# Performance work log

Hardware: AMD Instinct MI355X
Metric: run time of the kernel (lower is better)

## Reference

```python
import jax, jax.numpy as jnp
import numpy as np

B, L, D_FEAT = 16, 2048, 512
H, D_HID, UNITS = 8, 512, 512


def setup_inputs() -> dict:
    key = jax.random.key(0)
    ks = jax.random.split(key, 8)
    s_feat = 1.0 / np.sqrt(D_FEAT)
    s_hid = 1.0 / np.sqrt(D_HID)
    s_u = 1.0 / np.sqrt(UNITS)
    return {
        "features": jax.random.normal(ks[0], (B, L, D_FEAT), jnp.float32),
        "hidden": jax.random.normal(ks[1], (B, H, D_HID), jnp.float32),
        # Per-head Dense params stacked along a leading head axis.
        "W1": jax.random.normal(ks[2], (H, D_FEAT, UNITS), jnp.float32) * s_feat,
        "b1": jnp.zeros((H, UNITS), jnp.float32),
        "W2": jax.random.normal(ks[3], (H, D_HID, UNITS), jnp.float32) * s_hid,
        "b2": jnp.zeros((H, UNITS), jnp.float32),
        "V": jax.random.normal(ks[4], (H, UNITS), jnp.float32) * s_u,
        "bV": jnp.zeros((H,), jnp.float32),
    }


def reference(features, hidden, W1, b1, W2, b2, V, bV):
    # features: [B, L, Df]; hidden: [B, H, Dh]
    # Per-head: tanh(W1(features) + W2(hidden_h)) -> V -> softmax over L -> weighted sum.
    f_proj = jnp.einsum("bld,hdu->bhlu", features, W1) + b1[None, :, None, :]   # [B,H,L,U]
    h_proj = jnp.einsum("bhd,hdu->bhu", hidden, W2) + b2[None, :, :]            # [B,H,U]
    act = jnp.tanh(f_proj + h_proj[:, :, None, :])                               # [B,H,L,U]
    score = jnp.einsum("bhlu,hu->bhl", act, V) + bV[None, :, None]               # [B,H,L]
    attn = jax.nn.softmax(score, axis=-1)                                        # softmax over L
    context = jnp.einsum("bhl,bld->bhd", attn, features)                         # [B,H,Df]
    # Original stacks weights (each [B,L,1]) along axis=2 -> [B,L,H,1]
    attention_weights = jnp.transpose(attn, (0, 2, 1))[..., None]                # [B,L,H,1]
    return context, attention_weights
```

## Files before the change

### kernel.cpp

```cpp
#include <hip/hip_runtime.h>
#include <hip/hip_bf16.h>

#define B_ 16
#define L_ 2048
#define DF 512
#define H_ 8
#define DH 512
#define U_ 512

typedef unsigned short u16;
typedef __attribute__((ext_vector_type(8))) short bf16x8;
typedef __attribute__((ext_vector_type(4))) float f32x4;

__device__ __forceinline__ u16 f2bf(float x) {
  __hip_bfloat16 h = __float2bfloat16(x);
  u16 u;
  __builtin_memcpy(&u, &h, 2);
  return u;
}

__device__ __forceinline__ void load_lds16(const void* g, void* l) {
  __builtin_amdgcn_global_load_lds(
      (const __attribute__((address_space(1))) void*)g,
      (__attribute__((address_space(3))) void*)l, 16, 0, 0);
}

__device__ __forceinline__ float fast_tanh2(float x) {
  float e = __expf(2.f * x);
  return 1.f - __fdividef(2.f, e + 1.f);
}

__global__ __launch_bounds__(256) void convert_kernel(
    const float* __restrict__ F, u16* __restrict__ Abf,
    const float* __restrict__ W1, u16* __restrict__ W1T) {
  __shared__ float t[32][33];
  if (blockIdx.x < 16384) {
    size_t i = ((size_t)blockIdx.x * 256 + threadIdx.x) * 4;
    float4 v = *(const float4*)(F + i);
    ushort4 o;
    o.x = f2bf(v.x); o.y = f2bf(v.y); o.z = f2bf(v.z); o.w = f2bf(v.w);
    *(ushort4*)(Abf + i) = o;
  } else {
    int bid = blockIdx.x - 16384;
    int d0 = (bid & 15) * 32, u0 = ((bid >> 4) & 15) * 32, h = bid >> 8;
    const float* src = W1 + (size_t)h * DF * U_;
    u16* dst = W1T + (size_t)h * U_ * DF;
#pragma unroll
    for (int i = 0; i < 4; ++i) {
      int idx = threadIdx.x + i * 256;
      int r = idx >> 5, c = idx & 31;
      t[r][c] = src[(size_t)(d0 + r) * U_ + u0 + c];
    }
    __syncthreads();
#pragma unroll
    for (int i = 0; i < 4; ++i) {
      int idx = threadIdx.x + i * 256;
      int r = idx >> 5, c = idx & 31;
      dst[(size_t)(u0 + r) * DF + d0 + c] = f2bf(t[c][r]);
    }
  }
}

__global__ __launch_bounds__(128) void hproj_part_kernel(
    const float* __restrict__ hidden, const float* __restrict__ W2,
    float* __restrict__ partial) {
  int h = blockIdx.x;
  int u = blockIdx.y * 128 + threadIdx.x;
  int d0 = blockIdx.z * 64;
  __shared__ float hs[B_][64];
  for (int idx = threadIdx.x; idx < B_ * 64; idx += 128) {
    int b = idx >> 6, d = idx & 63;
    hs[b][d] = hidden[(size_t)(b * H_ + h) * DH + d0 + d];
  }
  __syncthreads();
  float acc[B_];
#pragma unroll
  for (int b = 0; b < B_; b++) acc[b] = 0.f;
  const float* w2p = W2 + ((size_t)h * DH + d0) * U_ + u;
  for (int d = 0; d < 64; d++) {
    float w = w2p[(size_t)d * U_];
#pragma unroll
    for (int b = 0; b < B_; b++) acc[b] += hs[b][d] * w;
  }
#pragma unroll
  for (int b = 0; b < B_; b++)
    partial[(((size_t)blockIdx.z * B_ + b) * H_ + h) * U_ + u] = acc[b];
}

__global__ __launch_bounds__(256) void hproj_combine_kernel(
    const float* __restrict__ partial, const float* __restrict__ b1,
    const float* __restrict__ b2, float* __restrict__ c) {
  int i = blockIdx.x * 256 + threadIdx.x;
  int hu = i & (H_ * U_ - 1);
  float s = b1[hu] + b2[hu];
#pragma unroll
  for (int z = 0; z < 8; z++) s += partial[(size_t)z * B_ * H_ * U_ + i];
  c[i] = s;
}

#define BKQ 32

__global__ __launch_bounds__(512, 2) void score_kernel(
    const u16* __restrict__ Abf, const u16* __restrict__ W1T,
    const float* __restrict__ C, const float* __restrict__ V,
    float* __restrict__ pscore) {
  int bid = blockIdx.x;
  int logical = (bid & 7) * 256 + (bid >> 3);
  int mt = logical >> 4;
  int hu = logical & 15;
  int h = hu & 7, ut = hu >> 3;
  int b = mt >> 3;
  int l0 = (mt & 7) * 256;
  int u0 = ut * 256;

  int tid = threadIdx.x;
  int lane = tid & 63, wid = tid >> 6;
  int wr = wid >> 2, wc = wid & 3;
  int rl = lane & 15, q = lane >> 4;

  __shared__ u16 As[4][256 * BKQ];
  __shared__ u16 Bs[4][256 * BKQ];
  __shared__ float redsm[4][256];

  const u16* Fb = Abf + ((size_t)b * L_ + l0) * DF;
  const u16* Wh = W1T + ((size_t)h * U_ + u0) * DF;

  float cu[4], vv[4];
#pragma unroll
  for (int n = 0; n < 4; ++n) {
    int col = u0 + wc * 64 + n * 16 + rl;
    cu[n] = C[(size_t)(b * H_ + h) * U_ + col];
    vv[n] = V[h * U_ + col];
  }
  f32x4 acc[8][4];
#pragma unroll
  for (int m = 0; m < 8; ++m)
#pragma unroll
    for (int n = 0; n < 4; ++n)
#pragma unroll
      for (int j = 0; j < 4; ++j) acc[m][n][j] = cu[n];

#define STAGE(bufi, kb)                                                    \
  {                                                                        \
    _Pragma("unroll") for (int i_ = 0; i_ < 2; ++i_) {                     \
      int idx_ = i_ * 512 + tid;                                           \
      int row_ = idx_ >> 2;                                                \
      int ke_ = ((idx_ & 3) ^ ((row_ >> 1) & 3)) << 3;                     \
      load_lds16(Fb + ((size_t)row_ << 9) + (kb) + ke_,                    \
                 &As[bufi][idx_ * 8]);                                     \
    }                                                                      \
    _Pragma("unroll") for (int i_ = 0; i_ < 2; ++i_) {                     \
      int idx_ = i_ * 512 + tid;                                           \
      int row_ = idx_ >> 2;                                                \
      int ke_ = ((idx_ & 3) ^ ((row_ >> 1) & 3)) << 3;                     \
      load_lds16(Wh + ((size_t)row_ << 9) + (kb) + ke_,                    \
                 &Bs[bufi][idx_ * 8]);                                     \
    }                                                                      \
  }

#define COMPUTE(bufi)                                                      \
  {                                                                        \
    bf16x8 bF[4];                                                          \
    _Pragma("unroll") for (int n = 0; n < 4; ++n) {                        \
      int rB = wc * 64 + n * 16 + rl;                                      \
      bF[n] = *(const bf16x8*)&Bs[bufi][(rB << 5) +                        \
                                        ((q ^ ((rB >> 1) & 3)) << 3)];     \
    }                                                                      \
    _Pragma("unroll") for (int m = 0; m < 8; ++m) {                        \
      int rA = wr * 128 + m * 16 + rl;                                     \
      bf16x8 aF = *(const bf16x8*)&As[bufi][(rA << 5) +                    \
                                           ((q ^ ((rA >> 1) & 3)) << 3)];  \
      _Pragma("unroll") for (int n = 0; n < 4; ++n)                        \
        acc[m][n] = __builtin_amdgcn_mfma_f32_16x16x32_bf16(               \
            aF, bF[n], acc[m][n], 0, 0, 0);                                \
    }                                                                      \
  }

  STAGE(0, 0);
  STAGE(1, BKQ);
  STAGE(2, 2 * BKQ);

#pragma unroll 1
  for (int t = 0; t < 13; ++t) {
    STAGE((t + 3) & 3, (t + 3) * BKQ);
    asm volatile("s_waitcnt vmcnt(12)" ::: "memory");
    __builtin_amdgcn_s_barrier();
    COMPUTE(t & 3);
    asm volatile("s_waitcnt lgkmcnt(0)" ::: "memory");
    __builtin_amdgcn_s_barrier();
  }
  asm volatile("s_waitcnt vmcnt(8)" ::: "memory");
  __builtin_amdgcn_s_barrier();
  COMPUTE(1);
  asm volatile("s_waitcnt lgkmcnt(0)" ::: "memory");
  __builtin_amdgcn_s_barrier();
  asm volatile("s_waitcnt vmcnt(4)" ::: "memory");
  __builtin_amdgcn_s_barrier();
  COMPUTE(2);
  asm volatile("s_waitcnt lgkmcnt(0)" ::: "memory");
  __builtin_amdgcn_s_barrier();
  asm volatile("s_waitcnt vmcnt(0)" ::: "memory");
  __builtin_amdgcn_s_barrier();
  COMPUTE(3);
#undef STAGE
#undef COMPUTE

  float part[32];
#pragma unroll
  for (int m = 0; m < 8; ++m)
#pragma unroll
    for (int j = 0; j < 4; ++j) {
      float s = 0.f;
#pragma unroll
      for (int n = 0; n < 4; ++n) s += fast_tanh2(acc[m][n][j]) * vv[n];
      part[m * 4 + j] = s;
    }
#pragma unroll
  for (int p = 0; p < 32; ++p) {
    float v = part[p];
    v += __shfl_xor(v, 1, 64);
    v += __shfl_xor(v, 2, 64);
    v += __shfl_xor(v, 4, 64);
    v += __shfl_xor(v, 8, 64);
    part[p] = v;
  }
  __syncthreads();
  if (rl == 0) {
#pragma unroll
    for (int m = 0; m < 8; ++m)
#pragma unroll
      for (int j = 0; j < 4; ++j)
        redsm[wc][wr * 128 + m * 16 + q * 4 + j] = part[m * 4 + j];
  }
  __syncthreads();
  if (tid < 256) {
    float s = redsm[0][tid] + redsm[1][tid] + redsm[2][tid] + redsm[3][tid];
    pscore[((size_t)ut * B_ * H_ + b * H_ + h) * L_ + l0 + tid] = s;
  }
}

__global__ __launch_bounds__(256) void softmax_kernel(
    const float* __restrict__ pscore, float* __restrict__ attn,
    float* __restrict__ aw_out) {
  int bh = blockIdx.x;
  int b = bh / H_, h = bh % H_;
  const float* p0 = pscore + (size_t)bh * L_;
  const float* p1 = pscore + ((size_t)B_ * H_ + bh) * L_;
  __shared__ float sv[L_];
  __shared__ float red[256];

  for (int i = threadIdx.x; i < L_ / 4; i += 256) {
    float4 a = ((const float4*)p0)[i];
    float4 c = ((const float4*)p1)[i];
    a.x += c.x; a.y += c.y; a.z += c.z; a.w += c.w;
    ((float4*)sv)[i] = a;
  }
  __syncthreads();

  float m = -1e30f;
  for (int l = threadIdx.x; l < L_; l += 256) m = fmaxf(m, sv[l]);
  red[threadIdx.x] = m;
  __syncthreads();
  for (int st = 128; st > 0; st >>= 1) {
    if (threadIdx.x < st)
      red[threadIdx.x] = fmaxf(red[threadIdx.x], red[threadIdx.x + st]);
    __syncthreads();
  }
  m = red[0];
  __syncthreads();

  float sum = 0.f;
  for (int l = threadIdx.x; l < L_; l += 256) sum += __expf(sv[l] - m);
  red[threadIdx.x] = sum;
  __syncthreads();
  for (int st = 128; st > 0; st >>= 1) {
    if (threadIdx.x < st) red[threadIdx.x] += red[threadIdx.x + st];
    __syncthreads();
  }
  float inv = 1.f / red[0];

  for (int l = threadIdx.x; l < L_; l += 256) {
    float a = __expf(sv[l] - m) * inv;
    attn[(size_t)bh * L_ + l] = a;
    aw_out[((size_t)b * L_ + l) * H_ + h] = a;
  }
}

__global__ __launch_bounds__(256) void context_part_kernel(
    const float* __restrict__ F, const float* __restrict__ attn,
    float* __restrict__ partial) {
  int b = blockIdx.x;
  int d0 = blockIdx.y * 64;
  int lz = blockIdx.z;
  int td = threadIdx.x & 63;
  int tl = threadIdx.x >> 6;

  __shared__ float as[H_][256];
  for (int idx = threadIdx.x; idx < H_ * 256; idx += 256)
    as[idx >> 8][idx & 255] =
        attn[((size_t)b * H_ + (idx >> 8)) * L_ + lz * 256 + (idx & 255)];
  __syncthreads();

  float acc[H_] = {};
  for (int l = tl; l < 256; l += 4) {
    float f = F[((size_t)b * L_ + lz * 256 + l) * DF + d0 + td];
#pragma unroll
    for (int h = 0; h < H_; h++) acc[h] += as[h][l] * f;
  }

  __shared__ float red[4][H_][64];
#pragma unroll
  for (int h = 0; h < H_; h++) red[tl][h][td] = acc[h];
  __syncthreads();
  if (tl == 0) {
#pragma unroll
    for (int h = 0; h < H_; h++) {
      float v = red[0][h][td] + red[1][h][td] + red[2][h][td] + red[3][h][td];
      partial[(size_t)lz * B_ * H_ * DF + ((size_t)b * H_ + h) * DF + d0 + td] =
          v;
    }
  }
}

__global__ __launch_bounds__(256) void context_combine_kernel(
    const float* __restrict__ partial, float* __restrict__ ctx_out) {
  int i = blockIdx.x * 256 + threadIdx.x;
  float s = 0.f;
#pragma unroll
  for (int z = 0; z < 8; z++) s += partial[(size_t)z * B_ * H_ * DF + i];
  ctx_out[i] = s;
}

extern "C" void kernel_launch(void* const* d_in, const int* in_sizes, int n_in,
                              void* d_out, int out_size, void* d_ws,
                              size_t ws_size, hipStream_t stream) {
  const float* features = (const float*)d_in[0];
  const float* hidden   = (const float*)d_in[1];
  const float* W1       = (const float*)d_in[2];
  const float* b1       = (const float*)d_in[3];
  const float* W2       = (const float*)d_in[4];
  const float* b2       = (const float*)d_in[5];
  const float* V        = (const float*)d_in[6];

  float* out = (float*)d_out;
  float* ctx_out = out;
  float* aw_out  = out + B_ * H_ * DF;

  float* c_buf  = (float*)d_ws;
  float* pscore = c_buf + (size_t)B_ * H_ * U_;
  float* attn   = pscore;
  float* hpart  = pscore;
  float* cpart  = pscore + (size_t)2 * B_ * H_ * L_;
  u16* Abf = (u16*)(cpart + (size_t)8 * B_ * H_ * DF);
  u16* W1T = Abf + (size_t)B_ * L_ * DF;

  convert_kernel<<<16384 + 2048, 256, 0, stream>>>(features, Abf, W1, W1T);
  hproj_part_kernel<<<dim3(H_, U_ / 128, 8), 128, 0, stream>>>(hidden, W2,
                                                               hpart);
  hproj_combine_kernel<<<(B_ * H_ * U_) / 256, 256, 0, stream>>>(hpart, b1, b2,
                                                                 c_buf);
  score_kernel<<<2048, 512, 0, stream>>>(Abf, W1T, c_buf, V, pscore);
  softmax_kernel<<<B_ * H_, 256, 0, stream>>>(pscore, attn, aw_out);
  context_part_kernel<<<dim3(B_, DF / 64, 8), 256, 0, stream>>>(features, attn,
                                                                cpart);
  context_combine_kernel<<<(B_ * H_ * DF) / 256, 256, 0, stream>>>(cpart,
                                                                   ctx_out);
}
```

Measured before the change: 268.7 us.

## Make score GEMM persistent with BK=64 double-buffered pipeline, fuse hproj into prep

The score kernel becomes persistent: 256 blocks each walk all eight L-tiles of one batch, head and U-half, using a BK=64 double-buffered LDS pipeline. Global-to-LDS loads are interleaved with MFMA quarter-steps, and the tanh/V reduction runs at each tile boundary. The hidden projection is merged into the conversion kernel to save a launch, and the context kernel reads the bf16 features instead of fp32 to halve its traffic. Risks: only 256 blocks, about one per CU, which may cut latency hiding; the context sum loses precision from the bf16 inputs.

```diff
diff --git a/kernel.cpp b/kernel.cpp
--- a/kernel.cpp
+++ b/kernel.cpp
@@ -19,6 +19,13 @@
   return u;
 }
 
+__device__ __forceinline__ float bf2f(u16 u) {
+  unsigned x = ((unsigned)u) << 16;
+  float f;
+  __builtin_memcpy(&f, &x, 4);
+  return f;
+}
+
 __device__ __forceinline__ void load_lds16(const void* g, void* l) {
   __builtin_amdgcn_global_load_lds(
       (const __attribute__((address_space(1))) void*)g,
@@ -30,17 +37,20 @@
   return 1.f - __fdividef(2.f, e + 1.f);
 }
 
-__global__ __launch_bounds__(256) void convert_kernel(
+__global__ __launch_bounds__(256) void prep_kernel(
     const float* __restrict__ F, u16* __restrict__ Abf,
-    const float* __restrict__ W1, u16* __restrict__ W1T) {
+    const float* __restrict__ W1, u16* __restrict__ W1T,
+    const float* __restrict__ hidden, const float* __restrict__ W2,
+    float* __restrict__ hpart) {
   __shared__ float t[32][33];
+  __shared__ float hs[B_][64];
   if (blockIdx.x < 16384) {
     size_t i = ((size_t)blockIdx.x * 256 + threadIdx.x) * 4;
     float4 v = *(const float4*)(F + i);
     ushort4 o;
     o.x = f2bf(v.x); o.y = f2bf(v.y); o.z = f2bf(v.z); o.w = f2bf(v.w);
     *(ushort4*)(Abf + i) = o;
-  } else {
+  } else if (blockIdx.x < 18432) {
     int bid = blockIdx.x - 16384;
     int d0 = (bid & 15) * 32, u0 = ((bid >> 4) & 15) * 32, h = bid >> 8;
     const float* src = W1 + (size_t)h * DF * U_;
@@ -58,33 +68,29 @@
       int r = idx >> 5, c = idx & 31;
       dst[(size_t)(u0 + r) * DF + d0 + c] = f2bf(t[c][r]);
     }
-  }
-}
-
-__global__ __launch_bounds__(128) void hproj_part_kernel(
-    const float* __restrict__ hidden, const float* __restrict__ W2,
-    float* __restrict__ partial) {
-  int h = blockIdx.x;
-  int u = blockIdx.y * 128 + threadIdx.x;
-  int d0 = blockIdx.z * 64;
-  __shared__ float hs[B_][64];
-  for (int idx = threadIdx.x; idx < B_ * 64; idx += 128) {
-    int b = idx >> 6, d = idx & 63;
-    hs[b][d] = hidden[(size_t)(b * H_ + h) * DH + d0 + d];
-  }
-  __syncthreads();
-  float acc[B_];
-#pragma unroll
-  for (int b = 0; b < B_; b++) acc[b] = 0.f;
-  const float* w2p = W2 + ((size_t)h * DH + d0) * U_ + u;
-  for (int d = 0; d < 64; d++) {
-    float w = w2p[(size_t)d * U_];
-#pragma unroll
-    for (int b = 0; b < B_; b++) acc[b] += hs[b][d] * w;
-  }
-#pragma unroll
-  for (int b = 0; b < B_; b++)
-    partial[(((size_t)blockIdx.z * B_ + b) * H_ + h) * U_ + u] = acc[b];
+  } else {
+    int bid = blockIdx.x - 18432;
+    int h = bid & 7, uy = (bid >> 3) & 1, dz = bid >> 4;
+    int u = uy * 256 + threadIdx.x;
+    int d0 = dz * 64;
+    for (int idx = threadIdx.x; idx < B_ * 64; idx += 256) {
+      int b = idx >> 6, d = idx & 63;
+      hs[b][d] = hidden[(size_t)(b * H_ + h) * DH + d0 + d];
+    }
+    __syncthreads();
+    float acc[B_];
+#pragma unroll
+    for (int b = 0; b < B_; b++) acc[b] = 0.f;
+    const float* w2p = W2 + ((size_t)h * DH + d0) * U_ + u;
+    for (int d = 0; d < 64; d++) {
+      float w = w2p[(size_t)d * U_];
+#pragma unroll
+      for (int b = 0; b < B_; b++) acc[b] += hs[b][d] * w;
+    }
+#pragma unroll
+    for (int b = 0; b < B_; b++)
+      hpart[(((size_t)dz * B_ + b) * H_ + h) * U_ + u] = acc[b];
+  }
 }
 
 __global__ __launch_bounds__(256) void hproj_combine_kernel(
@@ -98,19 +104,14 @@
   c[i] = s;
 }
 
-#define BKQ 32
-
 __global__ __launch_bounds__(512, 2) void score_kernel(
     const u16* __restrict__ Abf, const u16* __restrict__ W1T,
     const float* __restrict__ C, const float* __restrict__ V,
     float* __restrict__ pscore) {
   int bid = blockIdx.x;
-  int logical = (bid & 7) * 256 + (bid >> 3);
-  int mt = logical >> 4;
-  int hu = logical & 15;
-  int h = hu & 7, ut = hu >> 3;
-  int b = mt >> 3;
-  int l0 = (mt & 7) * 256;
+  int xcd = bid & 7, slot = bid >> 3;
+  int h = slot & 7, ut = (slot >> 3) & 1, mg = slot >> 4;
+  int b = xcd * 2 + mg;
   int u0 = ut * 256;
 
   int tid = threadIdx.x;
@@ -118,11 +119,11 @@
   int wr = wid >> 2, wc = wid & 3;
   int rl = lane & 15, q = lane >> 4;
 
-  __shared__ u16 As[4][256 * BKQ];
-  __shared__ u16 Bs[4][256 * BKQ];
+  __shared__ u16 As[2][256 * 64];
+  __shared__ u16 Bs[2][256 * 64];
   __shared__ float redsm[4][256];
 
-  const u16* Fb = Abf + ((size_t)b * L_ + l0) * DF;
+  const u16* FbB = Abf + (size_t)b * L_ * DF;
   const u16* Wh = W1T + ((size_t)h * U_ + u0) * DF;
 
   float cu[4], vv[4];
@@ -140,103 +141,136 @@
 #pragma unroll
       for (int j = 0; j < 4; ++j) acc[m][n][j] = cu[n];
 
-#define STAGE(bufi, kb)                                                    \
+#define SA_(bi, hf, l0v, kb)                                               \
   {                                                                        \
     _Pragma("unroll") for (int i_ = 0; i_ < 2; ++i_) {                     \
-      int idx_ = i_ * 512 + tid;                                           \
-      int row_ = idx_ >> 2;                                                \
-      int ke_ = ((idx_ & 3) ^ ((row_ >> 1) & 3)) << 3;                     \
-      load_lds16(Fb + ((size_t)row_ << 9) + (kb) + ke_,                    \
-                 &As[bufi][idx_ * 8]);                                     \
+      int idx_ = (hf)*1024 + i_ * 512 + tid;                               \
+      int row_ = idx_ >> 3;                                                \
+      int ke_ = ((idx_ & 7) ^ (row_ & 7)) << 3;                            \
+      load_lds16(FbB + (((size_t)((l0v) + row_)) << 9) + (kb) + ke_,       \
+                 &As[bi][idx_ * 8]);                                       \
     }                                                                      \
+  }
+#define SB_(bi, hf, kb)                                                    \
+  {                                                                        \
     _Pragma("unroll") for (int i_ = 0; i_ < 2; ++i_) {                     \
-      int idx_ = i_ * 512 + tid;                                           \
-      int row_ = idx_ >> 2;                                                \
-      int ke_ = ((idx_ & 3) ^ ((row_ >> 1) & 3)) << 3;                     \
-      load_lds16(Wh + ((size_t)row_ << 9) + (kb) + ke_,                    \
-                 &Bs[bufi][idx_ * 8]);                                     \
+      int idx_ = (hf)*1024 + i_ * 512 + tid;                               \
+      int row_ = idx_ >> 3;                                                \
+      int ke_ = ((idx_ & 7) ^ (row_ & 7)) << 3;                            \
+      load_lds16(Wh + (((size_t)row_) << 9) + (kb) + ke_,                  \
+                 &Bs[bi][idx_ * 8]);                                       \
     }                                                                      \
   }
-
-#define COMPUTE(bufi)                                                      \
+#define RD_A(mh, ks, bi)                                                   \
   {                                                                        \
-    bf16x8 bF[4];                                                          \
-    _Pragma("unroll") for (int n = 0; n < 4; ++n) {                        \
-      int rB = wc * 64 + n * 16 + rl;                                      \
-      bF[n] = *(const bf16x8*)&Bs[bufi][(rB << 5) +                        \
-                                        ((q ^ ((rB >> 1) & 3)) << 3)];     \
+    _Pragma("unroll") for (int mm = 0; mm < 4; ++mm) {                     \
+      int rA = wr * 128 + ((mh)*4 + mm) * 16 + rl;                         \
+      aF[mm] = *(const bf16x8*)&As[bi][(rA << 6) +                         \
+                                       ((((ks)*4 + q) ^ (rA & 7)) << 3)];  \
     }                                                                      \
-    _Pragma("unroll") for (int m = 0; m < 8; ++m) {                        \
-      int rA = wr * 128 + m * 16 + rl;                                     \
-      bf16x8 aF = *(const bf16x8*)&As[bufi][(rA << 5) +                    \
-                                           ((q ^ ((rA >> 1) & 3)) << 3)];  \
-      _Pragma("unroll") for (int n = 0; n < 4; ++n)                        \
-        acc[m][n] = __builtin_amdgcn_mfma_f32_16x16x32_bf16(               \
-            aF, bF[n], acc[m][n], 0, 0, 0);                                \
+  }
+#define RD_B(ks, bi)                                                       \
+  {                                                                        \
+    _Pragma("unroll") for (int nn = 0; nn < 4; ++nn) {                     \
+      int rB = wc * 64 + nn * 16 + rl;                                     \
+      bF[nn] = *(const bf16x8*)&Bs[bi][(rB << 6) +                         \
+                                       ((((ks)*4 + q) ^ (rB & 7)) << 3)];  \
     }                                                                      \
   }
-
-  STAGE(0, 0);
-  STAGE(1, BKQ);
-  STAGE(2, 2 * BKQ);
+#define MMQ(mh)                                                            \
+  {                                                                        \
+    _Pragma("unroll") for (int mm = 0; mm < 4; ++mm)                       \
+    _Pragma("unroll") for (int nn = 0; nn < 4; ++nn)                       \
+      acc[(mh)*4 + mm][nn] = __builtin_amdgcn_mfma_f32_16x16x32_bf16(      \
+          aF[mm], bF[nn], acc[(mh)*4 + mm][nn], 0, 0, 0);                  \
+  }
+
+  SA_(0, 0, 0, 0);
+  SB_(0, 0, 0);
+  SB_(0, 1, 0);
+  SA_(0, 1, 0, 0);
+  asm volatile("s_waitcnt vmcnt(2)" ::: "memory");
+  __builtin_amdgcn_s_barrier();
+  __builtin_amdgcn_sched_barrier(0);
 
 #pragma unroll 1
-  for (int t = 0; t < 13; ++t) {
-    STAGE((t + 3) & 3, (t + 3) * BKQ);
-    asm volatile("s_waitcnt vmcnt(12)" ::: "memory");
+  for (int g = 0; g < 64; ++g) {
+    int cc = g & 1, nb = cc ^ 1;
+    int l0 = (g >> 3) * 256;
+    int l0n = ((g + 1) >> 3) * 256;
+    int kbn = ((g + 1) & 7) * 64;
+    bf16x8 aF[4], bF[4];
+    RD_A(0, 0, cc);
+    RD_B(0, cc);
+    if (g < 63) SA_(nb, 0, l0n, kbn);
+    MMQ(0);
+    if (g < 63)
+      asm volatile("s_waitcnt vmcnt(2)" ::: "memory");
+    else
+      asm volatile("s_waitcnt vmcnt(0)" ::: "memory");
     __builtin_amdgcn_s_barrier();
-    COMPUTE(t & 3);
+    __builtin_amdgcn_sched_barrier(0);
+    RD_A(1, 0, cc);
+    if (g < 63) SB_(nb, 0, kbn);
+    MMQ(1);
+    RD_A(0, 1, cc);
+    RD_B(1, cc);
+    if (g < 63) SB_(nb, 1, kbn);
+    MMQ(0);
+    RD_A(1, 1, cc);
+    if (g < 63) SA_(nb, 1, l0n, kbn);
+    MMQ(1);
     asm volatile("s_waitcnt lgkmcnt(0)" ::: "memory");
+    asm volatile("s_waitcnt vmcnt(2)" ::: "memory");
     __builtin_amdgcn_s_barrier();
-  }
-  asm volatile("s_waitcnt vmcnt(8)" ::: "memory");
-  __builtin_amdgcn_s_barrier();
-  COMPUTE(1);
-  asm volatile("s_waitcnt lgkmcnt(0)" ::: "memory");
-  __builtin_amdgcn_s_barrier();
-  asm volatile("s_waitcnt vmcnt(4)" ::: "memory");
-  __builtin_amdgcn_s_barrier();
-  COMPUTE(2);
-  asm volatile("s_waitcnt lgkmcnt(0)" ::: "memory");
-  __builtin_amdgcn_s_barrier();
-  asm volatile("s_waitcnt vmcnt(0)" ::: "memory");
-  __builtin_amdgcn_s_barrier();
-  COMPUTE(3);
-#undef STAGE
-#undef COMPUTE
-
-  float part[32];
-#pragma unroll
-  for (int m = 0; m < 8; ++m)
-#pragma unroll
-    for (int j = 0; j < 4; ++j) {
-      float s = 0.f;
-#pragma unroll
-      for (int n = 0; n < 4; ++n) s += fast_tanh2(acc[m][n][j]) * vv[n];
-      part[m * 4 + j] = s;
-    }
-#pragma unroll
-  for (int p = 0; p < 32; ++p) {
-    float v = part[p];
-    v += __shfl_xor(v, 1, 64);
-    v += __shfl_xor(v, 2, 64);
-    v += __shfl_xor(v, 4, 64);
-    v += __shfl_xor(v, 8, 64);
-    part[p] = v;
-  }
-  __syncthreads();
-  if (rl == 0) {
-#pragma unroll
-    for (int m = 0; m < 8; ++m)
-#pragma unroll
-      for (int j = 0; j < 4; ++j)
-        redsm[wc][wr * 128 + m * 16 + q * 4 + j] = part[m * 4 + j];
-  }
-  __syncthreads();
-  if (tid < 256) {
-    float s = redsm[0][tid] + redsm[1][tid] + redsm[2][tid] + redsm[3][tid];
-    pscore[((size_t)ut * B_ * H_ + b * H_ + h) * L_ + l0 + tid] = s;
-  }
+    __builtin_amdgcn_sched_barrier(0);
+    if ((g & 7) == 7) {
+      float part[32];
+#pragma unroll
+      for (int m = 0; m < 8; ++m)
+#pragma unroll
+        for (int j = 0; j < 4; ++j) {
+          float s = 0.f;
+#pragma unroll
+          for (int n = 0; n < 4; ++n) s += fast_tanh2(acc[m][n][j]) * vv[n];
+          part[m * 4 + j] = s;
+        }
+#pragma unroll
+      for (int p = 0; p < 32; ++p) {
+        float v = part[p];
+        v += __shfl_xor(v, 1, 64);
+        v += __shfl_xor(v, 2, 64);
+        v += __shfl_xor(v, 4, 64);
+        v += __shfl_xor(v, 8, 64);
+        part[p] = v;
+      }
+      __syncthreads();
+      if (rl == 0) {
+#pragma unroll
+        for (int m = 0; m < 8; ++m)
+#pragma unroll
+          for (int j = 0; j < 4; ++j)
+            redsm[wc][wr * 128 + m * 16 + q * 4 + j] = part[m * 4 + j];
+      }
+      __syncthreads();
+      if (tid < 256) {
+        float s = redsm[0][tid] + redsm[1][tid] + redsm[2][tid] +
+                  redsm[3][tid];
+        pscore[((size_t)ut * B_ * H_ + b * H_ + h) * L_ + l0 + tid] = s;
+      }
+#pragma unroll
+      for (int m = 0; m < 8; ++m)
+#pragma unroll
+        for (int n = 0; n < 4; ++n)
+#pragma unroll
+          for (int j = 0; j < 4; ++j) acc[m][n][j] = cu[n];
+    }
+  }
+#undef SA_
+#undef SB_
+#undef RD_A
+#undef RD_B
+#undef MMQ
 }
 
 __global__ __launch_bounds__(256) void softmax_kernel(
@@ -287,7 +321,7 @@
 }
 
 __global__ __launch_bounds__(256) void context_part_kernel(
-    const float* __restrict__ F, const float* __restrict__ attn,
+    const u16* __restrict__ Abf, const float* __restrict__ attn,
     float* __restrict__ partial) {
   int b = blockIdx.x;
   int d0 = blockIdx.y * 64;
@@ -303,7 +337,7 @@
 
   float acc[H_] = {};
   for (int l = tl; l < 256; l += 4) {
-    float f = F[((size_t)b * L_ + lz * 256 + l) * DF + d0 + td];
+    float f = bf2f(Abf[((size_t)b * L_ + lz * 256 + l) * DF + d0 + td]);
 #pragma unroll
     for (int h = 0; h < H_; h++) acc[h] += as[h][l] * f;
   }
@@ -354,14 +388,13 @@
   u16* Abf = (u16*)(cpart + (size_t)8 * B_ * H_ * DF);
   u16* W1T = Abf + (size_t)B_ * L_ * DF;
 
-  convert_kernel<<<16384 + 2048, 256, 0, stream>>>(features, Abf, W1, W1T);
-  hproj_part_kernel<<<dim3(H_, U_ / 128, 8), 128, 0, stream>>>(hidden, W2,
-                                                               hpart);
+  prep_kernel<<<16384 + 2048 + 128, 256, 0, stream>>>(features, Abf, W1, W1T,
+                                                      hidden, W2, hpart);
   hproj_combine_kernel<<<(B_ * H_ * U_) / 256, 256, 0, stream>>>(hpart, b1, b2,
                                                                  c_buf);
-  score_kernel<<<2048, 512, 0, stream>>>(Abf, W1T, c_buf, V, pscore);
+  score_kernel<<<256, 512, 0, stream>>>(Abf, W1T, c_buf, V, pscore);
   softmax_kernel<<<B_ * H_, 256, 0, stream>>>(pscore, attn, aw_out);
-  context_part_kernel<<<dim3(B_, DF / 64, 8), 256, 0, stream>>>(features, attn,
+  context_part_kernel<<<dim3(B_, DF / 64, 8), 256, 0, stream>>>(Abf, attn,
                                                                 cpart);
   context_combine_kernel<<<(B_ * H_ * DF) / 256, 256, 0, stream>>>(cpart,
                                                                    ctx_out);
```

After: 239.0 us. -11.1%, faster.
